# Performance work log

Measured on AMD Instinct MI355X. Metric: run time of the kernel, lower is better.

Reference implementation:

```python
import jax, jax.numpy as jnp
import numpy as np

NU = 0.01
N = 8192
HID = 256
NMID = 9  # nine 256x256 hidden layers between the first (2->256) and last (256->1)


def softplus100(x):
    # torch.nn.Softplus(beta=100): (1/beta)*log(1+exp(beta*x)); jax.nn.softplus is stable
    return jax.nn.softplus(100.0 * x) / 100.0


def mlp(pt, W0, b0, Wm, bm, Wl, bl):
    # pt: (2,) -> scalar
    h = softplus100(pt @ W0 + b0)
    for i in range(NMID):
        h = softplus100(h @ Wm[i] + bm[i])
    return (h @ Wl + bl)[0]


def setup_inputs() -> dict:
    key = jax.random.key(0)
    ks = jax.random.split(key, 12)

    def init_net(k):
        kk = jax.random.split(k, 3)
        return {
            'W0': jax.random.normal(kk[0], (2, HID)) / jnp.sqrt(2.0),
            'b0': jnp.zeros((HID,)),
            'Wm': jax.random.normal(kk[1], (NMID, HID, HID)) / jnp.sqrt(float(HID)),
            'bm': jnp.zeros((NMID, HID)),
            'Wl': jax.random.normal(kk[2], (HID, 1)) / jnp.sqrt(float(HID)),
            'bl': jnp.zeros((1,)),
        }

    psi = init_net(ks[0])
    pnet = init_net(ks[1])
    inp = {
        'x': jax.random.uniform(ks[2], (N, 1)),
        'y': jax.random.uniform(ks[3], (N, 1)),
        'u': jax.random.normal(ks[4], (N, 1)),
        'v': jax.random.normal(ks[5], (N, 1)),
        'p': jax.random.normal(ks[6], (N, 1)),
        'bc_mask': jax.random.randint(ks[7], (N,), 0, 2).astype(bool),
    }
    for prefix, net in (('psi', psi), ('p', pnet)):
        for name, val in net.items():
            inp[f'{prefix}_{name}'] = val
    return inp


def reference(x, y, u, v, p, bc_mask,
              psi_W0, psi_b0, psi_Wm, psi_bm, psi_Wl, psi_bl,
              p_W0, p_b0, p_Wm, p_bm, p_Wl, p_bl):
    xy = jnp.concatenate([x, y], axis=1)  # (N, 2)

    def psi_fn(pt):
        return mlp(pt, psi_W0, psi_b0, psi_Wm, psi_bm, psi_Wl, psi_bl)

    def p_fn(pt):
        return mlp(pt, p_W0, p_b0, p_Wm, p_bm, p_Wl, p_bl)

    def per_point(pt):
        g = jax.grad(psi_fn)(pt)                         # (2,)   psi_x, psi_y
        Hm = jax.jacfwd(jax.grad(psi_fn))(pt)            # (2,2)  psi_ij
        T = jax.jacfwd(jax.jacfwd(jax.grad(psi_fn)))(pt) # (2,2,2) psi_ijk
        pv = p_fn(pt)
        gp = jax.grad(p_fn)(pt)                          # (2,)   p_x, p_y
        return g, Hm, T, pv, gp

    g, Hm, T, pv, gp = jax.vmap(per_point)(xy)

    u_pred = g[:, 1]          # u = dpsi/dy
    v_pred = -g[:, 0]         # v = -dpsi/dx
    u_x = Hm[:, 1, 0]
    u_y = Hm[:, 1, 1]
    v_x = -Hm[:, 0, 0]
    v_y = -Hm[:, 0, 1]
    u_xx = T[:, 1, 0, 0]
    u_yy = T[:, 1, 1, 1]
    v_xx = -T[:, 0, 0, 0]
    v_yy = -T[:, 0, 1, 1]
    p_x = gp[:, 0]
    p_y = gp[:, 1]

    f_u = 2 * u_pred * u_x + u_pred * v_y + v_pred * u_y + p_x - NU * (u_xx + u_yy)
    f_v = 2 * v_pred * v_y + u_pred * v_x + v_pred * u_x + p_y - NU * (v_xx + v_yy)

    ut, vt, pt_ = u[:, 0], v[:, 0], p[:, 0]
    m = bc_mask.astype(u_pred.dtype)
    ms = jnp.maximum(jnp.sum(m), 1.0)

    def masked_mse(a, b):
        return jnp.sum(m * (a - b) ** 2) / ms

    def mse(a, b):
        return jnp.mean((a - b) ** 2)

    u_bc = masked_mse(ut, u_pred)
    v_bc = masked_mse(vt, v_pred)
    p_bc = masked_mse(pt_, pv)
    u_tr = mse(ut, u_pred)
    v_tr = mse(vt, v_pred)
    p_tr = mse(pt_, pv)
    rans = jnp.mean(f_u ** 2) + jnp.mean(f_v ** 2)

    psi_loss = u_bc + v_bc + rans
    p_loss = p_bc + rans
    return (psi_loss, p_loss, u_tr, v_tr, p_tr, rans)
```

## Files before the change

### kernel.cpp

```cpp
#include <hip/hip_runtime.h>
#include <hip/hip_bf16.h>
#include <math.h>

#define HIDDEN 256
#define NPTS 8192
#define NMID_L 9
#define NU_C 0.01f

typedef __attribute__((ext_vector_type(8))) short bf16x8;
typedef __attribute__((ext_vector_type(4))) float floatx4;
typedef __attribute__((ext_vector_type(4))) unsigned uintx4;

__device__ __forceinline__ ushort f2b(float a) {
    unsigned x = __float_as_uint(a);
    return (ushort)((x + 0x7fffu + ((x >> 16) & 1u)) >> 16);
}
__device__ __forceinline__ float b2f(ushort u) {
    return __uint_as_float(((unsigned)u) << 16);
}
__device__ __forceinline__ void split2(float a, ushort& hi, ushort& lo) {
    ushort h = f2b(a);
    lo = f2b(a - b2f(h));
    hi = h;
}
__device__ __forceinline__ unsigned packsplit(float a) {
    ushort h = f2b(a);
    ushort l = f2b(a - b2f(h));
    return ((unsigned)h << 16) | (unsigned)l;
}

__device__ __forceinline__ void act_derivs(float z, float& h, float& s1, float& s2, float& s3)
{
    float t = 100.0f * z;
    float at = fabsf(t);
    float e = __expf(-at);
    float r = __builtin_amdgcn_rcpf(1.0f + e);
    float a_ = e * r;
    bool pos = (t >= 0.0f);
    float s   = pos ? r  : a_;
    float oms = pos ? a_ : r;
    float sp = fmaxf(t, 0.0f) - __logf(r);
    h  = 0.01f * sp;
    s1 = s;
    s2 = 100.0f * s * oms;
    s3 = s2 * (100.0f - 200.0f * s);
}

__global__ __launch_bounds__(256) void wprep(const float* __restrict__ psi_Wm,
                                             const float* __restrict__ p_Wm,
                                             ushort* __restrict__ Wfh, ushort* __restrict__ Wfl)
{
    int bid = blockIdx.x;
    int l = bid >> 4;
    int tile = bid & 15;
    int tk = (tile >> 2) * 64;
    int tn = (tile & 3) * 64;
    const float* W = (l < 9) ? (psi_Wm + (size_t)l * 65536)
                             : (p_Wm + (size_t)(l - 9) * 65536);
    __shared__ float tileS[64][65];
    int t = threadIdx.x;
    #pragma unroll
    for (int i = 0; i < 16; ++i) {
        int r = i * 4 + (t >> 6);
        int c = t & 63;
        tileS[r][c] = W[(size_t)(tk + r) * HIDDEN + tn + c];
    }
    __syncthreads();
    bf16x8* oh = (bf16x8*)Wfh;
    bf16x8* ol = (bf16x8*)Wfl;
    #pragma unroll
    for (int i = 0; i < 2; ++i) {
        int g = i * 256 + t;
        int n_loc = g >> 3;
        int kg = g & 7;
        int n = tn + n_loc;
        int k0 = tk + kg * 8;
        int w = n >> 5, tt = (n >> 4) & 1, col = n & 15;
        int ch = k0 >> 5, ks = (k0 >> 3) & 3;
        size_t fidx = ((((size_t)l * 8 + w) * 2 + tt) * 8 + ch) * 64 + ks * 16 + col;
        bf16x8 vh, vl;
        #pragma unroll
        for (int e = 0; e < 8; ++e) {
            ushort hh, ll;
            split2(tileS[kg * 8 + e][n_loc], hh, ll);
            vh[e] = (short)hh;
            vl[e] = (short)ll;
        }
        oh[fidx] = vh;
        ol[fidx] = vl;
    }
}

template<int C, int DF, int DN, int PB, bool ADDBL>
__global__ __launch_bounds__(512, 2) void fused_net(
    const float* __restrict__ x, const float* __restrict__ y,
    const float* __restrict__ W0, const float* __restrict__ b0,
    const ushort* __restrict__ Wfh, const ushort* __restrict__ Wfl,
    const float* __restrict__ bm,
    const float* __restrict__ Wl, const float* __restrict__ bl,
    float* __restrict__ P)
{
    extern __shared__ char smem[];
    const int t = threadIdx.x;
    const int lane = t & 63;
    const int wv = t >> 6;
    const int p0 = blockIdx.x * 16;
    const int lp = lane & 15;
    const int kg = lane >> 4;

    {
        float xx = x[p0 + lp];
        float yy = y[p0 + lp];
        unsigned pk[C][8];
        #pragma unroll
        for (int e = 0; e < 8; ++e) {
            int j = wv * 32 + kg * 8 + e;
            float ax = W0[j];
            float ay = W0[HIDDEN + j];
            float a = xx * ax + yy * ay + b0[j];
            float h, s1, s2, s3;
            act_derivs(a, h, s1, s2, s3);
            float vals[C];
            vals[0] = h; vals[1] = s1 * ax; vals[2] = s1 * ay;
            if constexpr (C == 10) {
                vals[3] = s2 * ax * ax;
                vals[4] = s2 * ax * ay;
                vals[5] = s2 * ay * ay;
                vals[6] = s3 * ax * ax * ax;
                vals[7] = s3 * ax * ax * ay;
                vals[8] = s3 * ax * ay * ay;
                vals[9] = s3 * ay * ay * ay;
            }
            #pragma unroll
            for (int c = 0; c < C; ++c) pk[c][e] = packsplit(vals[c]);
        }
        #pragma unroll
        for (int c = 0; c < C; ++c) {
            char* R = smem + (c * 8 + wv) * 2048 + lp * 128;
            uintx4 q0 = {pk[c][0], pk[c][1], pk[c][2], pk[c][3]};
            uintx4 q1 = {pk[c][4], pk[c][5], pk[c][6], pk[c][7]};
            *(uintx4*)(R + (((kg * 2 + 0) + lp) & 7) * 16) = q0;
            *(uintx4*)(R + (((kg * 2 + 1) + lp) & 7) * 16) = q1;
        }
    }
    __syncthreads();

    const bf16x8* WfhV = (const bf16x8*)Wfh;
    const bf16x8* WflV = (const bf16x8*)Wfl;

    for (int l = 0; l < NMID_L; ++l) {
        floatx4 acc[C][2];
        #pragma unroll
        for (int c = 0; c < C; ++c) {
            acc[c][0] = (floatx4){0.f, 0.f, 0.f, 0.f};
            acc[c][1] = (floatx4){0.f, 0.f, 0.f, 0.f};
        }
        const size_t wbase = ((size_t)l * 8 + wv) * 1024;
        #pragma unroll
        for (int ch = 0; ch < 8; ++ch) {
            bf16x8 bh[2], blo[2];
            #pragma unroll
            for (int tt = 0; tt < 2; ++tt) {
                size_t bi = wbase + ((size_t)tt * 8 + ch) * 64 + lane;
                bh[tt] = WfhV[bi];
                blo[tt] = WflV[bi];
            }
            const int sw0 = (((kg * 2 + 0) + lp) & 7) * 16;
            const int sw1 = (((kg * 2 + 1) + lp) & 7) * 16;
            #pragma unroll
            for (int c = 0; c < C; ++c) {
                const char* R = smem + (c * 8 + ch) * 2048 + lp * 128;
                uintx4 u0 = *(const uintx4*)(R + sw0);
                uintx4 u1 = *(const uintx4*)(R + sw1);
                uintx4 hu, lu;
                hu[0] = __builtin_amdgcn_perm(u0[1], u0[0], 0x07060302u);
                hu[1] = __builtin_amdgcn_perm(u0[3], u0[2], 0x07060302u);
                hu[2] = __builtin_amdgcn_perm(u1[1], u1[0], 0x07060302u);
                hu[3] = __builtin_amdgcn_perm(u1[3], u1[2], 0x07060302u);
                lu[0] = __builtin_amdgcn_perm(u0[1], u0[0], 0x05040100u);
                lu[1] = __builtin_amdgcn_perm(u0[3], u0[2], 0x05040100u);
                lu[2] = __builtin_amdgcn_perm(u1[1], u1[0], 0x05040100u);
                lu[3] = __builtin_amdgcn_perm(u1[3], u1[2], 0x05040100u);
                bf16x8 ah = __builtin_bit_cast(bf16x8, hu);
                bf16x8 al = __builtin_bit_cast(bf16x8, lu);
                #pragma unroll
                for (int tt = 0; tt < 2; ++tt) {
                    acc[c][tt] = __builtin_amdgcn_mfma_f32_16x16x32_bf16(ah, bh[tt], acc[c][tt], 0, 0, 0);
                    acc[c][tt] = __builtin_amdgcn_mfma_f32_16x16x32_bf16(ah, blo[tt], acc[c][tt], 0, 0, 0);
                    acc[c][tt] = __builtin_amdgcn_mfma_f32_16x16x32_bf16(al, bh[tt], acc[c][tt], 0, 0, 0);
                }
            }
        }
        __syncthreads();

        float bb[2];
        bb[0] = bm[l * 256 + wv * 32 + lp];
        bb[1] = bm[l * 256 + wv * 32 + 16 + lp];
        float hv[2][4], s1v[2][4], s2v[2][4], s3v[2][4];
        #pragma unroll
        for (int tt = 0; tt < 2; ++tt)
        #pragma unroll
        for (int r = 0; r < 4; ++r) {
            float z = acc[0][tt][r] + bb[tt];
            act_derivs(z, hv[tt][r], s1v[tt][r], s2v[tt][r], s3v[tt][r]);
        }

        #pragma unroll
        for (int c = 0; c < C; ++c) {
            char* R = smem + (c * 8 + wv) * 2048;
            #pragma unroll
            for (int tt = 0; tt < 2; ++tt)
            #pragma unroll
            for (int r = 0; r < 4; ++r) {
                float s1 = s1v[tt][r], s2 = s2v[tt][r], s3 = s3v[tt][r];
                float ax = acc[1][tt][r], ay = acc[2][tt][r];
                float val;
                if (c == 0) val = hv[tt][r];
                else if (c == 1) val = s1 * ax;
                else if (c == 2) val = s1 * ay;
                else if constexpr (C == 10) {
                    float axx = acc[3][tt][r], axy = acc[4][tt][r], ayy = acc[5][tt][r];
                    float axxx = acc[6][tt][r], axxy = acc[7][tt][r];
                    float axyy = acc[8][tt][r], ayyy = acc[9][tt][r];
                    if (c == 3) val = s2 * ax * ax + s1 * axx;
                    else if (c == 4) val = s2 * ax * ay + s1 * axy;
                    else if (c == 5) val = s2 * ay * ay + s1 * ayy;
                    else if (c == 6) val = s3 * ax * ax * ax + 3.f * s2 * ax * axx + s1 * axxx;
                    else if (c == 7) val = s3 * ax * ax * ay + s2 * (2.f * ax * axy + ay * axx) + s1 * axxy;
                    else if (c == 8) val = s3 * ax * ay * ay + s2 * (2.f * ay * axy + ax * ayy) + s1 * axyy;
                    else val = s3 * ay * ay * ay + 3.f * s2 * ay * ayy + s1 * ayyy;
                } else val = 0.f;
                int p = (kg << 2) + r;
                int kk = tt * 16 + lp;
                int sw = ((kk >> 2) + p) & 7;
                *(unsigned*)(R + p * 128 + sw * 16 + (kk & 3) * 4) = packsplit(val);
            }
        }
        __syncthreads();
    }

    {
        float4 w0 = ((const float4*)Wl)[wv * 8 + kg * 2];
        float4 w1 = ((const float4*)Wl)[wv * 8 + kg * 2 + 1];
        float part[DN];
        #pragma unroll
        for (int i = 0; i < DN; ++i) {
            int c = DF + i;
            const char* R = smem + (c * 8 + wv) * 2048 + lp * 128;
            uintx4 u0 = *(const uintx4*)(R + (((kg * 2 + 0) + lp) & 7) * 16);
            uintx4 u1 = *(const uintx4*)(R + (((kg * 2 + 1) + lp) & 7) * 16);
            float s = 0.f;
            #pragma unroll
            for (int e = 0; e < 4; ++e)
                s += (b2f((ushort)(u0[e] >> 16)) + b2f((ushort)(u0[e] & 0xffffu))) * (&w0.x)[e];
            #pragma unroll
            for (int e = 0; e < 4; ++e)
                s += (b2f((ushort)(u1[e] >> 16)) + b2f((ushort)(u1[e] & 0xffffu))) * (&w1.x)[e];
            s += __shfl_xor(s, 16, 64);
            s += __shfl_xor(s, 32, 64);
            part[i] = s;
        }
        __syncthreads();
        if (lane < 16) {
            float* sc = (float*)(smem + wv * 2048);
            #pragma unroll
            for (int i = 0; i < DN; ++i) sc[i * 16 + lane] = part[i];
        }
        __syncthreads();
        if (t < 16 * DN) {
            int p = t & 15, i = t >> 4;
            float s = 0.f;
            #pragma unroll
            for (int w = 0; w < 8; ++w)
                s += ((const float*)(smem + w * 2048))[i * 16 + p];
            if (ADDBL && i == 0) s += bl[0];
            P[(size_t)(p0 + p) * 16 + PB + i] = s;
        }
    }
}

__global__ __launch_bounds__(256) void loss_partials(
    const float* __restrict__ P, const float* __restrict__ u,
    const float* __restrict__ v, const float* __restrict__ pr,
    const int* __restrict__ mask, float* __restrict__ partials)
{
    int i = blockIdx.x * 256 + threadIdx.x;
    float s[9];
    #pragma unroll
    for (int k = 0; k < 9; ++k) s[k] = 0.f;
    if (i < NPTS) {
        const float* Pi = P + (size_t)i * 16;
        float psix = Pi[0], psiy = Pi[1], psixx = Pi[2], psixy = Pi[3], psiyy = Pi[4];
        float psixxx = Pi[5], psixxy = Pi[6], psixyy = Pi[7], psiyyy = Pi[8];
        float pv = Pi[9], ppx = Pi[10], ppy = Pi[11];
        float up = psiy, vp = -psix;
        float u_x = psixy, u_y = psiyy, v_x = -psixx, v_y = -psixy;
        float u_xx = psixxy, u_yy = psiyyy, v_xx = -psixxx, v_yy = -psixyy;
        float f_u = 2.f * up * u_x + up * v_y + vp * u_y + ppx - NU_C * (u_xx + u_yy);
        float f_v = 2.f * vp * v_y + up * v_x + vp * u_x + ppy - NU_C * (v_xx + v_yy);
        float ut = u[i], vt = v[i], pt = pr[i];
        float m = mask[i] ? 1.f : 0.f;
        float du = ut - up, dv = vt - vp, dp = pt - pv;
        s[0] = m * du * du; s[1] = m * dv * dv; s[2] = m * dp * dp;
        s[3] = du * du;     s[4] = dv * dv;     s[5] = dp * dp;
        s[6] = f_u * f_u;   s[7] = f_v * f_v;   s[8] = m;
    }
    int lane = threadIdx.x & 63, wid = threadIdx.x >> 6;
    __shared__ float red[4][9];
    #pragma unroll
    for (int k = 0; k < 9; ++k) {
        float xv = s[k];
        #pragma unroll
        for (int off = 32; off; off >>= 1) xv += __shfl_down(xv, off, 64);
        s[k] = xv;
    }
    if (lane == 0) {
        #pragma unroll
        for (int k = 0; k < 9; ++k) red[wid][k] = s[k];
    }
    __syncthreads();
    if (threadIdx.x == 0) {
        #pragma unroll
        for (int k = 0; k < 9; ++k)
            partials[blockIdx.x * 9 + k] = red[0][k] + red[1][k] + red[2][k] + red[3][k];
    }
}

__global__ void loss_final(const float* __restrict__ partials, float* __restrict__ out)
{
    int lane = threadIdx.x;
    float sums[9];
    #pragma unroll
    for (int k = 0; k < 9; ++k) {
        float xv = (lane < 32) ? partials[lane * 9 + k] : 0.f;
        #pragma unroll
        for (int off = 32; off; off >>= 1) xv += __shfl_down(xv, off, 64);
        sums[k] = xv;
    }
    if (lane == 0) {
        float ms = fmaxf(sums[8], 1.0f);
        float inv_n = 1.0f / (float)NPTS;
        float u_bc = sums[0] / ms, v_bc = sums[1] / ms, p_bc = sums[2] / ms;
        float u_tr = sums[3] * inv_n, v_tr = sums[4] * inv_n, p_tr = sums[5] * inv_n;
        float rans = sums[6] * inv_n + sums[7] * inv_n;
        out[0] = u_bc + v_bc + rans;
        out[1] = p_bc + rans;
        out[2] = u_tr;
        out[3] = v_tr;
        out[4] = p_tr;
        out[5] = rans;
    }
}

extern "C" void kernel_launch(void* const* d_in, const int* in_sizes, int n_in,
                              void* d_out, int out_size, void* d_ws, size_t ws_size,
                              hipStream_t stream)
{
    (void)in_sizes; (void)n_in; (void)out_size; (void)ws_size;
    const float* x    = (const float*)d_in[0];
    const float* y    = (const float*)d_in[1];
    const float* u    = (const float*)d_in[2];
    const float* v    = (const float*)d_in[3];
    const float* pr   = (const float*)d_in[4];
    const int*   mask = (const int*)d_in[5];
    const float* psi_W0 = (const float*)d_in[6];
    const float* psi_b0 = (const float*)d_in[7];
    const float* psi_Wm = (const float*)d_in[8];
    const float* psi_bm = (const float*)d_in[9];
    const float* psi_Wl = (const float*)d_in[10];
    const float* psi_bl = (const float*)d_in[11];
    const float* p_W0 = (const float*)d_in[12];
    const float* p_b0 = (const float*)d_in[13];
    const float* p_Wm = (const float*)d_in[14];
    const float* p_bm = (const float*)d_in[15];
    const float* p_Wl = (const float*)d_in[16];
    const float* p_bl = (const float*)d_in[17];

    float*  P        = (float*)d_ws;
    float*  partials = P + (size_t)NPTS * 16;
    ushort* Wfh      = (ushort*)(partials + 512);
    ushort* Wfl      = Wfh + (size_t)18 * 65536;

    wprep<<<288, 256, 0, stream>>>(psi_Wm, p_Wm, Wfh, Wfl);

    fused_net<10, 1, 9, 0, false><<<NPTS / 16, 512, 10 * 16384, stream>>>(
        x, y, psi_W0, psi_b0, Wfh, Wfl, psi_bm, psi_Wl, psi_bl, P);

    fused_net<3, 0, 3, 9, true><<<NPTS / 16, 512, 3 * 16384, stream>>>(
        x, y, p_W0, p_b0, Wfh + (size_t)9 * 65536, Wfl + (size_t)9 * 65536,
        p_bm, p_Wl, p_bl, P);

    loss_partials<<<NPTS / 256, 256, 0, stream>>>(P, u, v, pr, mask, partials);
    loss_final<<<1, 64, 0, stream>>>(partials, (float*)d_out);
}
```

Measured before the change: 471.5 us.

## Swap MFMA operand roles and relayout activations for transposed accumulator output

Weights now feed the MFMA A operand and activations the B operand, so each lane's accumulator holds consecutive output features rather than consecutive points. The activation tiles in shared memory are relaid with a permuted k ordering (kappa_of), which lets the epilogue write packed uint2 pairs and lets the matmul read contiguous 32-byte rows without swizzle arithmetic. The weight-prep kernel reads global weights directly in this permuted order, with no shared-memory transpose. This is meant to cut LDS store count and address math in the per-layer epilogue. It risks bank conflicts in the unswizzled layout, and the prep kernel now does strided global reads.

```diff
diff --git a/kernel.cpp b/kernel.cpp
--- a/kernel.cpp
+++ b/kernel.cpp
@@ -27,6 +27,10 @@
     ushort h = f2b(a);
     ushort l = f2b(a - b2f(h));
     return ((unsigned)h << 16) | (unsigned)l;
+}
+
+__device__ __forceinline__ int kappa_of(int kgg, int ep) {
+    return 16 * (kgg >> 1) + 4 * (ep >> 1) + 2 * (kgg & 1) + (ep & 1);
 }
 
 __device__ __forceinline__ void act_derivs(float z, float& h, float& s1, float& s2, float& s3)
@@ -51,41 +55,30 @@
                                              ushort* __restrict__ Wfh, ushort* __restrict__ Wfl)
 {
     int bid = blockIdx.x;
-    int l = bid >> 4;
-    int tile = bid & 15;
-    int tk = (tile >> 2) * 64;
-    int tn = (tile & 3) * 64;
+    int l = bid >> 3, wv = bid & 7;
     const float* W = (l < 9) ? (psi_Wm + (size_t)l * 65536)
                              : (p_Wm + (size_t)(l - 9) * 65536);
-    __shared__ float tileS[64][65];
     int t = threadIdx.x;
-    #pragma unroll
-    for (int i = 0; i < 16; ++i) {
-        int r = i * 4 + (t >> 6);
-        int c = t & 63;
-        tileS[r][c] = W[(size_t)(tk + r) * HIDDEN + tn + c];
-    }
-    __syncthreads();
+    int lane = t & 63;
+    int m = lane & 15, kgg = lane >> 4;
+    int grp = t >> 6;
     bf16x8* oh = (bf16x8*)Wfh;
     bf16x8* ol = (bf16x8*)Wfl;
     #pragma unroll
-    for (int i = 0; i < 2; ++i) {
-        int g = i * 256 + t;
-        int n_loc = g >> 3;
-        int kg = g & 7;
-        int n = tn + n_loc;
-        int k0 = tk + kg * 8;
-        int w = n >> 5, tt = (n >> 4) & 1, col = n & 15;
-        int ch = k0 >> 5, ks = (k0 >> 3) & 3;
-        size_t fidx = ((((size_t)l * 8 + w) * 2 + tt) * 8 + ch) * 64 + ks * 16 + col;
+    for (int gi = 0; gi < 4; ++gi) {
+        int gid = grp * 4 + gi;
+        int tt = gid >> 3, ch = gid & 7;
+        int n = wv * 32 + tt * 16 + m;
         bf16x8 vh, vl;
         #pragma unroll
-        for (int e = 0; e < 8; ++e) {
+        for (int ep = 0; ep < 8; ++ep) {
+            int k = ch * 32 + kappa_of(kgg, ep);
             ushort hh, ll;
-            split2(tileS[kg * 8 + e][n_loc], hh, ll);
-            vh[e] = (short)hh;
-            vl[e] = (short)ll;
-        }
+            split2(W[(size_t)k * HIDDEN + n], hh, ll);
+            vh[ep] = (short)hh;
+            vl[ep] = (short)ll;
+        }
+        size_t fidx = ((((size_t)l * 8 + wv) * 2 + tt) * 8 + ch) * 64 + lane;
         oh[fidx] = vh;
         ol[fidx] = vl;
     }
@@ -111,36 +104,39 @@
     {
         float xx = x[p0 + lp];
         float yy = y[p0 + lp];
-        unsigned pk[C][8];
-        #pragma unroll
-        for (int e = 0; e < 8; ++e) {
-            int j = wv * 32 + kg * 8 + e;
-            float ax = W0[j];
-            float ay = W0[HIDDEN + j];
-            float a = xx * ax + yy * ay + b0[j];
-            float h, s1, s2, s3;
-            act_derivs(a, h, s1, s2, s3);
-            float vals[C];
-            vals[0] = h; vals[1] = s1 * ax; vals[2] = s1 * ay;
-            if constexpr (C == 10) {
-                vals[3] = s2 * ax * ax;
-                vals[4] = s2 * ax * ay;
-                vals[5] = s2 * ay * ay;
-                vals[6] = s3 * ax * ax * ax;
-                vals[7] = s3 * ax * ax * ay;
-                vals[8] = s3 * ax * ay * ay;
-                vals[9] = s3 * ay * ay * ay;
-            }
-            #pragma unroll
-            for (int c = 0; c < C; ++c) pk[c][e] = packsplit(vals[c]);
-        }
-        #pragma unroll
-        for (int c = 0; c < C; ++c) {
-            char* R = smem + (c * 8 + wv) * 2048 + lp * 128;
-            uintx4 q0 = {pk[c][0], pk[c][1], pk[c][2], pk[c][3]};
-            uintx4 q1 = {pk[c][4], pk[c][5], pk[c][6], pk[c][7]};
-            *(uintx4*)(R + (((kg * 2 + 0) + lp) & 7) * 16) = q0;
-            *(uintx4*)(R + (((kg * 2 + 1) + lp) & 7) * 16) = q1;
+        #pragma unroll
+        for (int e = 0; e < 8; e += 2) {
+            float vals2[C][2];
+            #pragma unroll
+            for (int ee = 0; ee < 2; ++ee) {
+                int j = wv * 32 + kg * 8 + e + ee;
+                float ax = W0[j];
+                float ay = W0[HIDDEN + j];
+                float a = xx * ax + yy * ay + b0[j];
+                float h, s1, s2, s3;
+                act_derivs(a, h, s1, s2, s3);
+                vals2[0][ee] = h; vals2[1][ee] = s1 * ax; vals2[2][ee] = s1 * ay;
+                if constexpr (C == 10) {
+                    vals2[3][ee] = s2 * ax * ax;
+                    vals2[4][ee] = s2 * ax * ay;
+                    vals2[5][ee] = s2 * ay * ay;
+                    vals2[6][ee] = s3 * ax * ax * ax;
+                    vals2[7][ee] = s3 * ax * ax * ay;
+                    vals2[8][ee] = s3 * ax * ay * ay;
+                    vals2[9][ee] = s3 * ay * ay * ay;
+                }
+            }
+            int kap = kg * 8 + e;
+            int kgg = 2 * (kap >> 4) + ((kap >> 1) & 1);
+            int ep  = 2 * ((kap >> 2) & 3);
+            #pragma unroll
+            for (int c = 0; c < C; ++c) {
+                char* R = smem + (c * 8 + wv) * 2048;
+                uint2 q;
+                q.x = packsplit(vals2[c][0]);
+                q.y = packsplit(vals2[c][1]);
+                *(uint2*)(R + (lp + 16 * kgg) * 32 + ep * 4) = q;
+            }
         }
     }
     __syncthreads();
@@ -158,20 +154,18 @@
         const size_t wbase = ((size_t)l * 8 + wv) * 1024;
         #pragma unroll
         for (int ch = 0; ch < 8; ++ch) {
-            bf16x8 bh[2], blo[2];
+            bf16x8 wah[2], wal[2];
             #pragma unroll
             for (int tt = 0; tt < 2; ++tt) {
                 size_t bi = wbase + ((size_t)tt * 8 + ch) * 64 + lane;
-                bh[tt] = WfhV[bi];
-                blo[tt] = WflV[bi];
-            }
-            const int sw0 = (((kg * 2 + 0) + lp) & 7) * 16;
-            const int sw1 = (((kg * 2 + 1) + lp) & 7) * 16;
+                wah[tt] = WfhV[bi];
+                wal[tt] = WflV[bi];
+            }
             #pragma unroll
             for (int c = 0; c < C; ++c) {
-                const char* R = smem + (c * 8 + ch) * 2048 + lp * 128;
-                uintx4 u0 = *(const uintx4*)(R + sw0);
-                uintx4 u1 = *(const uintx4*)(R + sw1);
+                const char* R = smem + (c * 8 + ch) * 2048 + lane * 32;
+                uintx4 u0 = *(const uintx4*)R;
+                uintx4 u1 = *(const uintx4*)(R + 16);
                 uintx4 hu, lu;
                 hu[0] = __builtin_amdgcn_perm(u0[1], u0[0], 0x07060302u);
                 hu[1] = __builtin_amdgcn_perm(u0[3], u0[2], 0x07060302u);
@@ -181,33 +175,33 @@
                 lu[1] = __builtin_amdgcn_perm(u0[3], u0[2], 0x05040100u);
                 lu[2] = __builtin_amdgcn_perm(u1[1], u1[0], 0x05040100u);
                 lu[3] = __builtin_amdgcn_perm(u1[3], u1[2], 0x05040100u);
-                bf16x8 ah = __builtin_bit_cast(bf16x8, hu);
-                bf16x8 al = __builtin_bit_cast(bf16x8, lu);
+                bf16x8 sh = __builtin_bit_cast(bf16x8, hu);
+                bf16x8 sl = __builtin_bit_cast(bf16x8, lu);
                 #pragma unroll
                 for (int tt = 0; tt < 2; ++tt) {
-                    acc[c][tt] = __builtin_amdgcn_mfma_f32_16x16x32_bf16(ah, bh[tt], acc[c][tt], 0, 0, 0);
-                    acc[c][tt] = __builtin_amdgcn_mfma_f32_16x16x32_bf16(ah, blo[tt], acc[c][tt], 0, 0, 0);
-                    acc[c][tt] = __builtin_amdgcn_mfma_f32_16x16x32_bf16(al, bh[tt], acc[c][tt], 0, 0, 0);
+                    acc[c][tt] = __builtin_amdgcn_mfma_f32_16x16x32_bf16(wah[tt], sh, acc[c][tt], 0, 0, 0);
+                    acc[c][tt] = __builtin_amdgcn_mfma_f32_16x16x32_bf16(wah[tt], sl, acc[c][tt], 0, 0, 0);
+                    acc[c][tt] = __builtin_amdgcn_mfma_f32_16x16x32_bf16(wal[tt], sh, acc[c][tt], 0, 0, 0);
                 }
             }
         }
         __syncthreads();
 
-        float bb[2];
-        bb[0] = bm[l * 256 + wv * 32 + lp];
-        bb[1] = bm[l * 256 + wv * 32 + 16 + lp];
+        float4 bb[2];
+        bb[0] = ((const float4*)(bm + l * 256 + wv * 32))[kg];
+        bb[1] = ((const float4*)(bm + l * 256 + wv * 32 + 16))[kg];
         float hv[2][4], s1v[2][4], s2v[2][4], s3v[2][4];
         #pragma unroll
         for (int tt = 0; tt < 2; ++tt)
         #pragma unroll
         for (int r = 0; r < 4; ++r) {
-            float z = acc[0][tt][r] + bb[tt];
+            float z = acc[0][tt][r] + (&bb[tt].x)[r];
             act_derivs(z, hv[tt][r], s1v[tt][r], s2v[tt][r], s3v[tt][r]);
         }
 
         #pragma unroll
         for (int c = 0; c < C; ++c) {
-            char* R = smem + (c * 8 + wv) * 2048;
+            float ov[2][4];
             #pragma unroll
             for (int tt = 0; tt < 2; ++tt)
             #pragma unroll
@@ -230,32 +224,42 @@
                     else if (c == 8) val = s3 * ax * ay * ay + s2 * (2.f * ay * axy + ax * ayy) + s1 * axyy;
                     else val = s3 * ay * ay * ay + 3.f * s2 * ay * ayy + s1 * ayyy;
                 } else val = 0.f;
-                int p = (kg << 2) + r;
-                int kk = tt * 16 + lp;
-                int sw = ((kk >> 2) + p) & 7;
-                *(unsigned*)(R + p * 128 + sw * 16 + (kk & 3) * 4) = packsplit(val);
+                ov[tt][r] = val;
+            }
+            char* R = smem + (c * 8 + wv) * 2048;
+            #pragma unroll
+            for (int tt = 0; tt < 2; ++tt)
+            #pragma unroll
+            for (int rp = 0; rp < 2; ++rp) {
+                int kggp = 2 * tt + rp;
+                uint2 q;
+                q.x = packsplit(ov[tt][rp * 2 + 0]);
+                q.y = packsplit(ov[tt][rp * 2 + 1]);
+                *(uint2*)(R + (lp + 16 * kggp) * 32 + kg * 8) = q;
             }
         }
         __syncthreads();
     }
 
     {
-        float4 w0 = ((const float4*)Wl)[wv * 8 + kg * 2];
-        float4 w1 = ((const float4*)Wl)[wv * 8 + kg * 2 + 1];
+        float wlv[8];
+        #pragma unroll
+        for (int ep = 0; ep < 8; ++ep)
+            wlv[ep] = Wl[wv * 32 + kappa_of(kg, ep)];
         float part[DN];
         #pragma unroll
         for (int i = 0; i < DN; ++i) {
             int c = DF + i;
-            const char* R = smem + (c * 8 + wv) * 2048 + lp * 128;
-            uintx4 u0 = *(const uintx4*)(R + (((kg * 2 + 0) + lp) & 7) * 16);
-            uintx4 u1 = *(const uintx4*)(R + (((kg * 2 + 1) + lp) & 7) * 16);
+            const char* R = smem + (c * 8 + wv) * 2048 + lane * 32;
+            uintx4 u0 = *(const uintx4*)R;
+            uintx4 u1 = *(const uintx4*)(R + 16);
             float s = 0.f;
             #pragma unroll
             for (int e = 0; e < 4; ++e)
-                s += (b2f((ushort)(u0[e] >> 16)) + b2f((ushort)(u0[e] & 0xffffu))) * (&w0.x)[e];
+                s += (b2f((ushort)(u0[e] >> 16)) + b2f((ushort)(u0[e] & 0xffffu))) * wlv[e];
             #pragma unroll
             for (int e = 0; e < 4; ++e)
-                s += (b2f((ushort)(u1[e] >> 16)) + b2f((ushort)(u1[e] & 0xffffu))) * (&w1.x)[e];
+                s += (b2f((ushort)(u1[e] >> 16)) + b2f((ushort)(u1[e] & 0xffffu))) * wlv[4 + e];
             s += __shfl_xor(s, 16, 64);
             s += __shfl_xor(s, 32, 64);
             part[i] = s;
@@ -381,7 +385,7 @@
     ushort* Wfh      = (ushort*)(partials + 512);
     ushort* Wfl      = Wfh + (size_t)18 * 65536;
 
-    wprep<<<288, 256, 0, stream>>>(psi_Wm, p_Wm, Wfh, Wfl);
+    wprep<<<144, 256, 0, stream>>>(psi_Wm, p_Wm, Wfh, Wfl);
 
     fused_net<10, 1, 9, 0, false><<<NPTS / 16, 512, 10 * 16384, stream>>>(
         x, y, psi_W0, psi_b0, Wfh, Wfl, psi_bm, psi_Wl, psi_bl, P);
```

New measurement: 467.6 us. No clear change (-0.8%).
